# Performance work log

Hardware: AMD Instinct MI355X
Metric: run time of the kernel (lower is better)

Reference implementation:

```python
import jax, jax.numpy as jnp
import numpy as np

B, S, D, H = 8, 1024, 1024, 16
DH = D // H
LN_EPS = 1e-5


def setup_inputs() -> dict:
    key = jax.random.key(0)
    ks = jax.random.split(key, 12)
    lim = 1.0 / np.sqrt(D)
    u = lambda k, shp: jax.random.uniform(k, shp, jnp.float32, -lim, lim)
    return {
        "x": jax.random.normal(ks[0], (B, S, D), jnp.float32),
        "Wq": u(ks[1], (D, D)), "bq": u(ks[2], (D,)),
        "Wk": u(ks[3], (D, D)), "bk": u(ks[4], (D,)),
        "Wv": u(ks[5], (D, D)), "bv": u(ks[6], (D,)),
        "Wo": u(ks[7], (D, D)), "bo": u(ks[8], (D,)),
        "gamma": jnp.ones((D,), jnp.float32),
        "beta": jnp.zeros((D,), jnp.float32),
        "num_head": H,
    }


def reference(x, Wq, bq, Wk, bk, Wv, bv, Wo, bo, gamma, beta, num_head):
    b, s, d = x.shape
    dh = d // num_head
    # projections (torch Linear: y = x @ W.T + b)
    Q = x @ Wq.T + bq
    K = x @ Wk.T + bk
    V = x @ Wv.T + bv
    # faithful raw row-major reshape [B, S, D] -> [B*H, S, DH] (as in the
    # original .view, which does NOT do a proper head split/transpose)
    Q = Q.reshape(b * num_head, -1, dh)
    K = K.reshape(b * num_head, -1, dh)
    V = V.reshape(b * num_head, -1, dh)
    scale = dh ** (-0.5)
    scores = jnp.einsum('bqd,bkd->bqk', Q, K) * scale  # [B*H, S, S]
    alpha = jax.nn.softmax(scores, axis=-1)
    context = jnp.einsum('bqk,bkd->bqd', alpha, V)
    context = context.reshape(b, -1, dh * num_head)
    out = context @ Wo.T + bo
    # dropout is identity in eval mode
    out = out + x
    mu = jnp.mean(out, axis=-1, keepdims=True)
    var = jnp.var(out, axis=-1, keepdims=True)
    out = (out - mu) * jax.lax.rsqrt(var + LN_EPS) * gamma + beta
    return out, alpha
```

## Files before the change

kernel.cpp:

```cpp
#include <hip/hip_runtime.h>
#include <stdint.h>
#include <math.h>

typedef __bf16 bf16_t;
typedef float f32x4 __attribute__((ext_vector_type(4)));
typedef __bf16 bf16x8 __attribute__((ext_vector_type(8)));
typedef __bf16 bf16x4 __attribute__((ext_vector_type(4)));

#define D_ 1024
#define M_ 8192

__device__ __forceinline__ f32x4 mfma16(bf16x8 a, bf16x8 b, f32x4 c) {
  return __builtin_amdgcn_mfma_f32_16x16x32_bf16(a, b, c, 0, 0, 0);
}

__device__ __forceinline__ void gl_lds16(const bf16_t* g, bf16_t* l) {
  __builtin_amdgcn_global_load_lds(
      (const __attribute__((address_space(1))) unsigned int*)g,
      (__attribute__((address_space(3))) unsigned int*)l, 16, 0, 0);
}

__global__ __launch_bounds__(256) void cvt_all(
    const float* __restrict__ x,
    const float* __restrict__ w0, const float* __restrict__ w1,
    const float* __restrict__ w2, const float* __restrict__ w3,
    bf16_t* __restrict__ xb,
    bf16_t* __restrict__ d0, bf16_t* __restrict__ d1,
    bf16_t* __restrict__ d2, bf16_t* __restrict__ d3) {
  int b = blockIdx.x;
  const float* s;
  bf16_t* d;
  int i;
  if (b < 4096) {
    s = x; d = xb; i = b * 256 + threadIdx.x;
  } else {
    int g = b - 4096;
    int which = g >> 9;
    s = which == 0 ? w0 : which == 1 ? w1 : which == 2 ? w2 : w3;
    d = which == 0 ? d0 : which == 1 ? d1 : which == 2 ? d2 : d3;
    i = (g & 511) * 256 + threadIdx.x;
  }
  const f32x4* p = (const f32x4*)(s + (size_t)i * 8);
  f32x4 a = p[0], bb = p[1];
  bf16x8 o;
  o[0] = (bf16_t)a.x; o[1] = (bf16_t)a.y; o[2] = (bf16_t)a.z; o[3] = (bf16_t)a.w;
  o[4] = (bf16_t)bb.x; o[5] = (bf16_t)bb.y; o[6] = (bf16_t)bb.z; o[7] = (bf16_t)bb.w;
  *(bf16x8*)(d + (size_t)i * 8) = o;
}

#define LDSB(e) (*(const bf16x8*)(Sm + (e)))

#define STG2(b, kt)                                                          \
  {                                                                          \
    _Pragma("unroll") for (int c = 0; c < 4; ++c) {                          \
      gl_lds16(A + (size_t)(m0 + c * 64 + srow) * 1024 + (kt) * 64 + scol,   \
               Sm + (b) * 32768 + c * 4096 + tid * 8);                       \
      gl_lds16(Wsel + (size_t)(n0 + c * 64 + srow) * 1024 + (kt) * 64 + scol,\
               Sm + (b) * 32768 + 16384 + c * 4096 + tid * 8);               \
    }                                                                        \
  }

__global__ __launch_bounds__(512) void gemm_qkv2(
    const bf16_t* __restrict__ A,
    const bf16_t* __restrict__ Wq, const bf16_t* __restrict__ Wk,
    const bf16_t* __restrict__ Wv,
    const float* __restrict__ bq, const float* __restrict__ bk,
    const float* __restrict__ bv,
    bf16_t* __restrict__ Oq, bf16_t* __restrict__ Ok, bf16_t* __restrict__ Ov) {
  __shared__ bf16_t Sm[65536];

  const int tid = threadIdx.x;
  const int l = tid & 63, w = tid >> 6;
  const int wm = w >> 2, wn = w & 3;
  const int lr = l & 15, lg = l >> 4;

  int wg = blockIdx.x;
  int xcd = wg & 7, local = wg >> 3;
  int bm = xcd * 4 + (local & 3);
  int bnid = local >> 2;
  int which = bnid >> 2;
  const bf16_t* Wsel = which == 0 ? Wq : (which == 1 ? Wk : Wv);
  const float* bias = which == 0 ? bq : (which == 1 ? bk : bv);
  bf16_t* O = which == 0 ? Oq : (which == 1 ? Ok : Ov);
  const float scale = which == 0 ? 0.18033688f : 1.0f;
  const int m0 = bm * 256, n0 = (bnid & 3) * 256;

  const int scol = ((l & 7) ^ ((l >> 3) & 7)) * 8;
  const int srow = w * 8 + (l >> 3);

  const int rdA = (wm * 128 + lr) * 64 + (lg ^ (lr & 7)) * 8;
  const int rdB = 16384 + (wn * 64 + lr) * 64 + (lg ^ (lr & 7)) * 8;

  f32x4 acc[8][4] = {};

  STG2(0, 0)
  asm volatile("s_waitcnt vmcnt(0)" ::: "memory");
  __builtin_amdgcn_sched_barrier(0);
  __builtin_amdgcn_s_barrier();

  int cur = 0;
  for (int kt = 0; kt < 16; ++kt) {
    if (kt < 15) STG2(cur ^ 1, kt + 1)
    const int bb = cur * 32768;
    bf16x8 bfr[4][2];
#pragma unroll
    for (int fn = 0; fn < 4; ++fn) {
      bfr[fn][0] = LDSB(bb + rdB + fn * 1024);
      bfr[fn][1] = LDSB((bb + rdB + fn * 1024) ^ 32);
    }
#pragma unroll
    for (int fm = 0; fm < 8; ++fm) {
      bf16x8 a0 = LDSB(bb + rdA + fm * 1024);
      bf16x8 a1 = LDSB((bb + rdA + fm * 1024) ^ 32);
#pragma unroll
      for (int fn = 0; fn < 4; ++fn) {
        acc[fm][fn] = mfma16(a0, bfr[fn][0], acc[fm][fn]);
        acc[fm][fn] = mfma16(a1, bfr[fn][1], acc[fm][fn]);
      }
    }
    asm volatile("s_waitcnt vmcnt(0)" ::: "memory");
    __builtin_amdgcn_sched_barrier(0);
    __builtin_amdgcn_s_barrier();
    cur ^= 1;
  }

#pragma unroll
  for (int fn = 0; fn < 4; ++fn) {
    int col = n0 + wn * 64 + fn * 16 + lr;
    float bb2 = bias[col];
#pragma unroll
    for (int fm = 0; fm < 8; ++fm) {
      int row = m0 + wm * 128 + fm * 16 + lg * 4;
      bf16_t* op = O + (size_t)row * 1024 + col;
#pragma unroll
      for (int r = 0; r < 4; ++r)
        op[(size_t)r * 1024] = (bf16_t)((acc[fm][fn][r] + bb2) * scale);
    }
  }
}

__device__ __forceinline__ void gemm_core(const bf16_t* __restrict__ A,
                                          const bf16_t* __restrict__ W,
                                          int m0, int n0,
                                          bf16_t* As, bf16_t* Bs,
                                          f32x4 acc[4][4]) {
  const int t = threadIdx.x;
  const int l = t & 63, w = t >> 6;
  const int wr = w >> 1, wc = w & 1;
  const int lr = l & 15, lg = l >> 4;
  const int srow = t >> 2;
  const int scol = (t & 3) * 8;
  const bf16_t* gA0 = A + (size_t)(m0 + srow) * D_ + scol;
  const bf16_t* gA1 = A + (size_t)(m0 + 64 + srow) * D_ + scol;
  const bf16_t* gB0 = W + (size_t)(n0 + srow) * D_ + scol;
  const bf16_t* gB1 = W + (size_t)(n0 + 64 + srow) * D_ + scol;

  for (int k0 = 0; k0 < D_; k0 += 32) {
    gl_lds16(gA0 + k0, As + t * 8);
    gl_lds16(gA1 + k0, As + 2048 + t * 8);
    gl_lds16(gB0 + k0, Bs + t * 8);
    gl_lds16(gB1 + k0, Bs + 2048 + t * 8);
    __syncthreads();
    bf16x8 af[4], bfr[4];
#pragma unroll
    for (int i = 0; i < 4; ++i)
      af[i] = *(const bf16x8*)(As + (wr * 64 + i * 16 + lr) * 32 + lg * 8);
#pragma unroll
    for (int i = 0; i < 4; ++i)
      bfr[i] = *(const bf16x8*)(Bs + (wc * 64 + i * 16 + lr) * 32 + lg * 8);
#pragma unroll
    for (int mi = 0; mi < 4; ++mi)
#pragma unroll
      for (int ni = 0; ni < 4; ++ni)
        acc[mi][ni] = mfma16(af[mi], bfr[ni], acc[mi][ni]);
    __syncthreads();
  }
}

__global__ __launch_bounds__(256) void gemm_proj(
    const bf16_t* __restrict__ A, const bf16_t* __restrict__ W,
    const float* __restrict__ bias, const float* __restrict__ xres,
    float* __restrict__ O) {
  __shared__ bf16_t As[128 * 32], Bs[128 * 32];
  int m0 = blockIdx.y * 128, n0 = blockIdx.x * 128;
  f32x4 acc[4][4] = {};
  gemm_core(A, W, m0, n0, As, Bs, acc);
  int t = threadIdx.x, l = t & 63, w = t >> 6;
  int wr = w >> 1, wc = w & 1, lr = l & 15, lg = l >> 4;
#pragma unroll
  for (int mi = 0; mi < 4; ++mi) {
#pragma unroll
    for (int ni = 0; ni < 4; ++ni) {
      int col = n0 + wc * 64 + ni * 16 + lr;
      float bb = bias[col];
      int row = m0 + wr * 64 + mi * 16 + lg * 4;
#pragma unroll
      for (int r = 0; r < 4; ++r) {
        size_t idx = (size_t)(row + r) * D_ + col;
        O[idx] = acc[mi][ni][r] + bb + xres[idx];
      }
    }
  }
}

__global__ __launch_bounds__(256) void transpose_v(const bf16_t* __restrict__ V,
                                                   bf16_t* __restrict__ Vt) {
  __shared__ float sT[128 * 33];
  int bh = blockIdx.x >> 3, st = blockIdx.x & 7;
  int s0 = st * 128;
  int t = threadIdx.x;
  const bf16_t* src = V + (size_t)bh * 65536 + (size_t)s0 * 64;
  int li = t >> 3, lc = t & 7;
#pragma unroll
  for (int p = 0; p < 4; ++p) {
    int row = p * 32 + li;
    f32x4 v = *(const f32x4*)(src + (size_t)row * 64 + lc * 8);
    float* dst = &sT[row * 33 + lc * 4];
    dst[0] = v[0]; dst[1] = v[1]; dst[2] = v[2]; dst[3] = v[3];
  }
  __syncthreads();
  int sc = t & 15, dh0 = t >> 4;
  bf16_t* dstb = Vt + (size_t)bh * 65536;
#pragma unroll
  for (int p = 0; p < 4; ++p) {
    int dh = dh0 + p * 16;
    bf16x8 o;
#pragma unroll
    for (int j = 0; j < 8; ++j) {
      int s = sc * 8 + j;
      o[j] = ((const bf16_t*)&sT[s * 33 + (dh >> 1)])[dh & 1];
    }
    *(bf16x8*)(dstb + (size_t)dh * 1024 + s0 + sc * 8) = o;
  }
}

#define SP_STRIDE 1064
__global__ __launch_bounds__(512, 4) void attn_kernel(
    const bf16_t* __restrict__ Q, const bf16_t* __restrict__ K,
    const bf16_t* __restrict__ Vt, float* __restrict__ alpha,
    bf16_t* __restrict__ ctx) {
  __shared__ bf16_t sP[32][SP_STRIDE];
  __shared__ float sRS[8][32];
  __shared__ float sL[32];

  int id = blockIdx.x;
  int g = id >> 3, x = id & 7;
  int qt = g & 31;
  int bh = ((g >> 5) << 3) | x;
  int q0 = qt * 32;

  const bf16_t* Qb = Q + (size_t)bh * 65536;
  const bf16_t* Kb = K + (size_t)bh * 65536;
  const bf16_t* Vb = Vt + (size_t)bh * 65536;
  float* Ab = alpha + (size_t)bh * 1048576 + (size_t)q0 * 1024;

  int t = threadIdx.x, l = t & 63, w = t >> 6;
  int lr = l & 15, lg = l >> 4;

  bf16x8 qa[2][2];
#pragma unroll
  for (int mi = 0; mi < 2; ++mi)
#pragma unroll
    for (int kk = 0; kk < 2; ++kk)
      qa[mi][kk] = *(const bf16x8*)(Qb + (size_t)(q0 + mi * 16 + lr) * 64 + kk * 32 + lg * 8);

  float pa0 = 0.f, pa1 = 0.f;
#pragma unroll
  for (int tt = 0; tt < 8; ++tt) {
    int n0 = w * 128 + tt * 16;
    bf16x8 kb0 = *(const bf16x8*)(Kb + (size_t)(n0 + lr) * 64 + lg * 8);
    bf16x8 kb1 = *(const bf16x8*)(Kb + (size_t)(n0 + lr) * 64 + 32 + lg * 8);
    f32x4 a0 = {0.f, 0.f, 0.f, 0.f};
    f32x4 a1 = {0.f, 0.f, 0.f, 0.f};
    a0 = mfma16(kb0, qa[0][0], a0);
    a0 = mfma16(kb1, qa[0][1], a0);
    a1 = mfma16(kb0, qa[1][0], a1);
    a1 = mfma16(kb1, qa[1][1], a1);
    bf16x4 w0, w1;
#pragma unroll
    for (int r = 0; r < 4; ++r) {
      float e0 = exp2f(a0[r]);
      float e1 = exp2f(a1[r]);
      pa0 += e0; pa1 += e1;
      w0[r] = (bf16_t)e0;
      w1[r] = (bf16_t)e1;
    }
    *(bf16x4*)&sP[lr][n0 + lg * 4] = w0;
    *(bf16x4*)&sP[16 + lr][n0 + lg * 4] = w1;
  }
  pa0 += __shfl_xor(pa0, 16); pa0 += __shfl_xor(pa0, 32);
  pa1 += __shfl_xor(pa1, 16); pa1 += __shfl_xor(pa1, 32);
  if (l < 16) {
    sRS[w][lr] = pa0;
    sRS[w][16 + lr] = pa1;
  }
  __syncthreads();
  if (t < 32) {
    float s = 0.f;
#pragma unroll
    for (int ww = 0; ww < 8; ++ww) s += sRS[ww][t];
    sL[t] = 1.0f / s;
  }
  __syncthreads();

  {
    int wm = w >> 2, wn = w & 3;
    f32x4 acc = {0.f, 0.f, 0.f, 0.f};
    const bf16_t* vp = Vb + (size_t)(wn * 16 + lr) * 1024 + lg * 8;
    const bf16_t* pp = &sP[wm * 16 + lr][lg * 8];
    int arow = t >> 4, acol = (t & 15) * 4;
    float inv = sL[arow];
    const bf16_t* ap = &sP[arow][acol];
    float* aout = Ab + (size_t)arow * 1024 + acol;
#pragma unroll 4
    for (int n0 = 0; n0 < 1024; n0 += 64) {
      bf16x8 ea0 = *(const bf16x8*)(pp + n0);
      bf16x8 vb0 = *(const bf16x8*)(vp + n0);
      acc = mfma16(ea0, vb0, acc);
      bf16x8 ea1 = *(const bf16x8*)(pp + n0 + 32);
      bf16x8 vb1 = *(const bf16x8*)(vp + n0 + 32);
      acc = mfma16(ea1, vb1, acc);
      bf16x4 p = *(const bf16x4*)(ap + n0);
      f32x4 o;
      o[0] = (float)p[0] * inv;
      o[1] = (float)p[1] * inv;
      o[2] = (float)p[2] * inv;
      o[3] = (float)p[3] * inv;
      __builtin_nontemporal_store(o, (f32x4*)(aout + n0));
    }
    bf16_t* cp = ctx + (size_t)bh * 65536 + (size_t)(q0 + wm * 16 + lg * 4) * 64 + wn * 16 + lr;
#pragma unroll
    for (int r = 0; r < 4; ++r)
      cp[(size_t)r * 64] = (bf16_t)(acc[r] * sL[wm * 16 + lg * 4 + r]);
  }
}

__global__ __launch_bounds__(256) void ln_kernel(float* __restrict__ io,
                                                 const float* __restrict__ gamma,
                                                 const float* __restrict__ beta) {
  int row = blockIdx.x;
  int t = threadIdx.x;
  float* p = io + (size_t)row * 1024;
  f32x4 v = *(const f32x4*)(p + t * 4);
  float s = v[0] + v[1] + v[2] + v[3];
  float s2 = v[0] * v[0] + v[1] * v[1] + v[2] * v[2] + v[3] * v[3];
#pragma unroll
  for (int off = 1; off <= 32; off <<= 1) {
    s += __shfl_xor(s, off);
    s2 += __shfl_xor(s2, off);
  }
  __shared__ float ps[4], ps2[4];
  int w = t >> 6, l = t & 63;
  if (l == 0) { ps[w] = s; ps2[w] = s2; }
  __syncthreads();
  float S = ps[0] + ps[1] + ps[2] + ps[3];
  float S2 = ps2[0] + ps2[1] + ps2[2] + ps2[3];
  float mu = S * (1.f / 1024.f);
  float var = S2 * (1.f / 1024.f) - mu * mu;
  float rs = rsqrtf(var + 1e-5f);
  f32x4 g = *(const f32x4*)(gamma + t * 4);
  f32x4 b = *(const f32x4*)(beta + t * 4);
  f32x4 o;
  o[0] = (v[0] - mu) * rs * g[0] + b[0];
  o[1] = (v[1] - mu) * rs * g[1] + b[1];
  o[2] = (v[2] - mu) * rs * g[2] + b[2];
  o[3] = (v[3] - mu) * rs * g[3] + b[3];
  *(f32x4*)(p + t * 4) = o;
}

extern "C" void kernel_launch(void* const* d_in, const int* in_sizes, int n_in,
                              void* d_out, int out_size, void* d_ws, size_t ws_size,
                              hipStream_t stream) {
  const float* x = (const float*)d_in[0];
  const float* Wq = (const float*)d_in[1];
  const float* bq = (const float*)d_in[2];
  const float* Wk = (const float*)d_in[3];
  const float* bk = (const float*)d_in[4];
  const float* Wv = (const float*)d_in[5];
  const float* bv = (const float*)d_in[6];
  const float* Wo = (const float*)d_in[7];
  const float* bo = (const float*)d_in[8];
  const float* gamma = (const float*)d_in[9];
  const float* beta = (const float*)d_in[10];

  char* ws = (char*)d_ws;
  size_t off = 0;
  bf16_t* xb = (bf16_t*)(ws + off);  off += (size_t)M_ * D_ * 2;
  bf16_t* Wqb = (bf16_t*)(ws + off); off += (size_t)D_ * D_ * 2;
  bf16_t* Wkb = (bf16_t*)(ws + off); off += (size_t)D_ * D_ * 2;
  bf16_t* Wvb = (bf16_t*)(ws + off); off += (size_t)D_ * D_ * 2;
  bf16_t* Wob = (bf16_t*)(ws + off); off += (size_t)D_ * D_ * 2;
  bf16_t* Qb = (bf16_t*)(ws + off);  off += (size_t)M_ * D_ * 2;
  bf16_t* Kb = (bf16_t*)(ws + off);  off += (size_t)M_ * D_ * 2;
  bf16_t* Vb = (bf16_t*)(ws + off);  off += (size_t)M_ * D_ * 2;
  bf16_t* Vtb = (bf16_t*)(ws + off); off += (size_t)M_ * D_ * 2;
  bf16_t* ctxb = (bf16_t*)(ws + off); off += (size_t)M_ * D_ * 2;

  float* out0 = (float*)d_out;
  float* alpha = out0 + (size_t)M_ * D_;

  cvt_all<<<6144, 256, 0, stream>>>(x, Wq, Wk, Wv, Wo, xb, Wqb, Wkb, Wvb, Wob);

  gemm_qkv2<<<384, 512, 0, stream>>>(xb, Wqb, Wkb, Wvb, bq, bk, bv, Qb, Kb, Vb);
  transpose_v<<<1024, 256, 0, stream>>>(Vb, Vtb);
  attn_kernel<<<4096, 512, 0, stream>>>(Qb, Kb, Vtb, alpha, ctxb);
  gemm_proj<<<dim3(8, 64), 256, 0, stream>>>(ctxb, Wob, bo, x, out0);
  ln_kernel<<<8192, 256, 0, stream>>>(out0, gamma, beta);
}
```

Measured before the change: 331.0 us.

## Share a 128x256 double-buffered GEMM core between QKV and output projection

The QKV GEMM tile shrinks from 256x256 to 128x256, doubling the grid to 768 workgroups and cutting LDS use and accumulator registers. The output projection moves off its simple single-buffered 128x128 kernel onto the same swizzled, double-buffered 128x256 core with XCD-aware block mapping, 512 threads and a 256-block grid. The aim is better CU occupancy and latency hiding in QKV and better load/compute overlap in the projection. In exchange, QKV re-reads the weight tiles more often per output.

```diff
diff --git a/kernel.cpp b/kernel.cpp
--- a/kernel.cpp
+++ b/kernel.cpp
@@ -50,15 +50,60 @@
 
 #define LDSB(e) (*(const bf16x8*)(Sm + (e)))
 
-#define STG2(b, kt)                                                          \
-  {                                                                          \
-    _Pragma("unroll") for (int c = 0; c < 4; ++c) {                          \
-      gl_lds16(A + (size_t)(m0 + c * 64 + srow) * 1024 + (kt) * 64 + scol,   \
-               Sm + (b) * 32768 + c * 4096 + tid * 8);                       \
-      gl_lds16(Wsel + (size_t)(n0 + c * 64 + srow) * 1024 + (kt) * 64 + scol,\
-               Sm + (b) * 32768 + 16384 + c * 4096 + tid * 8);               \
-    }                                                                        \
-  }
+#define STG26(b, kt)                                                          \
+  {                                                                           \
+    _Pragma("unroll") for (int c = 0; c < 2; ++c)                             \
+        gl_lds16(Ap + (size_t)(m0 + c * 64 + srow) * 1024 + (kt) * 64 + scol, \
+                 Sm + (b) * 24576 + c * 4096 + tid * 8);                      \
+    _Pragma("unroll") for (int c = 0; c < 4; ++c)                             \
+        gl_lds16(Bp + (size_t)(n0 + c * 64 + srow) * 1024 + (kt) * 64 + scol, \
+                 Sm + (b) * 24576 + 8192 + c * 4096 + tid * 8);               \
+  }
+
+__device__ __forceinline__ void core_128x256(const bf16_t* __restrict__ Ap,
+                                             const bf16_t* __restrict__ Bp,
+                                             int m0, int n0, bf16_t* Sm,
+                                             f32x4 acc[4][4]) {
+  const int tid = threadIdx.x;
+  const int l = tid & 63, w = tid >> 6;
+  const int wm = w >> 2, wn = w & 3;
+  const int lr = l & 15, lg = l >> 4;
+  const int scol = ((l & 7) ^ ((l >> 3) & 7)) * 8;
+  const int srow = tid >> 3;
+  const int rdA = (wm * 64 + lr) * 64 + (lg ^ (lr & 7)) * 8;
+  const int rdB = 8192 + (wn * 64 + lr) * 64 + (lg ^ (lr & 7)) * 8;
+
+  STG26(0, 0)
+  asm volatile("s_waitcnt vmcnt(0)" ::: "memory");
+  __builtin_amdgcn_sched_barrier(0);
+  __builtin_amdgcn_s_barrier();
+
+  int cur = 0;
+  for (int kt = 0; kt < 16; ++kt) {
+    if (kt < 15) STG26(cur ^ 1, kt + 1)
+    const int bb = cur * 24576;
+    bf16x8 bfr[4][2];
+#pragma unroll
+    for (int fn = 0; fn < 4; ++fn) {
+      bfr[fn][0] = LDSB(bb + rdB + fn * 1024);
+      bfr[fn][1] = LDSB((bb + rdB + fn * 1024) ^ 32);
+    }
+#pragma unroll
+    for (int fm = 0; fm < 4; ++fm) {
+      bf16x8 a0 = LDSB(bb + rdA + fm * 1024);
+      bf16x8 a1 = LDSB((bb + rdA + fm * 1024) ^ 32);
+#pragma unroll
+      for (int fn = 0; fn < 4; ++fn) {
+        acc[fm][fn] = mfma16(a0, bfr[fn][0], acc[fm][fn]);
+        acc[fm][fn] = mfma16(a1, bfr[fn][1], acc[fm][fn]);
+      }
+    }
+    asm volatile("s_waitcnt vmcnt(0)" ::: "memory");
+    __builtin_amdgcn_sched_barrier(0);
+    __builtin_amdgcn_s_barrier();
+    cur ^= 1;
+  }
+}
 
 __global__ __launch_bounds__(512) void gemm_qkv2(
     const bf16_t* __restrict__ A,
@@ -67,70 +112,33 @@
     const float* __restrict__ bq, const float* __restrict__ bk,
     const float* __restrict__ bv,
     bf16_t* __restrict__ Oq, bf16_t* __restrict__ Ok, bf16_t* __restrict__ Ov) {
-  __shared__ bf16_t Sm[65536];
-
-  const int tid = threadIdx.x;
-  const int l = tid & 63, w = tid >> 6;
-  const int wm = w >> 2, wn = w & 3;
-  const int lr = l & 15, lg = l >> 4;
+  __shared__ bf16_t Sm[49152];
 
   int wg = blockIdx.x;
   int xcd = wg & 7, local = wg >> 3;
-  int bm = xcd * 4 + (local & 3);
-  int bnid = local >> 2;
+  int bm = xcd * 8 + (local & 7);
+  int bnid = local >> 3;
   int which = bnid >> 2;
   const bf16_t* Wsel = which == 0 ? Wq : (which == 1 ? Wk : Wv);
   const float* bias = which == 0 ? bq : (which == 1 ? bk : bv);
   bf16_t* O = which == 0 ? Oq : (which == 1 ? Ok : Ov);
   const float scale = which == 0 ? 0.18033688f : 1.0f;
-  const int m0 = bm * 256, n0 = (bnid & 3) * 256;
-
-  const int scol = ((l & 7) ^ ((l >> 3) & 7)) * 8;
-  const int srow = w * 8 + (l >> 3);
-
-  const int rdA = (wm * 128 + lr) * 64 + (lg ^ (lr & 7)) * 8;
-  const int rdB = 16384 + (wn * 64 + lr) * 64 + (lg ^ (lr & 7)) * 8;
-
-  f32x4 acc[8][4] = {};
-
-  STG2(0, 0)
-  asm volatile("s_waitcnt vmcnt(0)" ::: "memory");
-  __builtin_amdgcn_sched_barrier(0);
-  __builtin_amdgcn_s_barrier();
-
-  int cur = 0;
-  for (int kt = 0; kt < 16; ++kt) {
-    if (kt < 15) STG2(cur ^ 1, kt + 1)
-    const int bb = cur * 32768;
-    bf16x8 bfr[4][2];
-#pragma unroll
-    for (int fn = 0; fn < 4; ++fn) {
-      bfr[fn][0] = LDSB(bb + rdB + fn * 1024);
-      bfr[fn][1] = LDSB((bb + rdB + fn * 1024) ^ 32);
-    }
-#pragma unroll
-    for (int fm = 0; fm < 8; ++fm) {
-      bf16x8 a0 = LDSB(bb + rdA + fm * 1024);
-      bf16x8 a1 = LDSB((bb + rdA + fm * 1024) ^ 32);
-#pragma unroll
-      for (int fn = 0; fn < 4; ++fn) {
-        acc[fm][fn] = mfma16(a0, bfr[fn][0], acc[fm][fn]);
-        acc[fm][fn] = mfma16(a1, bfr[fn][1], acc[fm][fn]);
-      }
-    }
-    asm volatile("s_waitcnt vmcnt(0)" ::: "memory");
-    __builtin_amdgcn_sched_barrier(0);
-    __builtin_amdgcn_s_barrier();
-    cur ^= 1;
-  }
-
+  const int m0 = bm * 128, n0 = (bnid & 3) * 256;
+
+  f32x4 acc[4][4] = {};
+  core_128x256(A, Wsel, m0, n0, Sm, acc);
+
+  const int tid = threadIdx.x;
+  const int l = tid & 63, w = tid >> 6;
+  const int wm = w >> 2, wn = w & 3;
+  const int lr = l & 15, lg = l >> 4;
 #pragma unroll
   for (int fn = 0; fn < 4; ++fn) {
     int col = n0 + wn * 64 + fn * 16 + lr;
     float bb2 = bias[col];
 #pragma unroll
-    for (int fm = 0; fm < 8; ++fm) {
-      int row = m0 + wm * 128 + fm * 16 + lg * 4;
+    for (int fm = 0; fm < 4; ++fm) {
+      int row = m0 + wm * 64 + fm * 16 + lg * 4;
       bf16_t* op = O + (size_t)row * 1024 + col;
 #pragma unroll
       for (int r = 0; r < 4; ++r)
@@ -139,65 +147,36 @@
   }
 }
 
-__device__ __forceinline__ void gemm_core(const bf16_t* __restrict__ A,
-                                          const bf16_t* __restrict__ W,
-                                          int m0, int n0,
-                                          bf16_t* As, bf16_t* Bs,
-                                          f32x4 acc[4][4]) {
-  const int t = threadIdx.x;
-  const int l = t & 63, w = t >> 6;
-  const int wr = w >> 1, wc = w & 1;
-  const int lr = l & 15, lg = l >> 4;
-  const int srow = t >> 2;
-  const int scol = (t & 3) * 8;
-  const bf16_t* gA0 = A + (size_t)(m0 + srow) * D_ + scol;
-  const bf16_t* gA1 = A + (size_t)(m0 + 64 + srow) * D_ + scol;
-  const bf16_t* gB0 = W + (size_t)(n0 + srow) * D_ + scol;
-  const bf16_t* gB1 = W + (size_t)(n0 + 64 + srow) * D_ + scol;
-
-  for (int k0 = 0; k0 < D_; k0 += 32) {
-    gl_lds16(gA0 + k0, As + t * 8);
-    gl_lds16(gA1 + k0, As + 2048 + t * 8);
-    gl_lds16(gB0 + k0, Bs + t * 8);
-    gl_lds16(gB1 + k0, Bs + 2048 + t * 8);
-    __syncthreads();
-    bf16x8 af[4], bfr[4];
-#pragma unroll
-    for (int i = 0; i < 4; ++i)
-      af[i] = *(const bf16x8*)(As + (wr * 64 + i * 16 + lr) * 32 + lg * 8);
-#pragma unroll
-    for (int i = 0; i < 4; ++i)
-      bfr[i] = *(const bf16x8*)(Bs + (wc * 64 + i * 16 + lr) * 32 + lg * 8);
-#pragma unroll
-    for (int mi = 0; mi < 4; ++mi)
-#pragma unroll
-      for (int ni = 0; ni < 4; ++ni)
-        acc[mi][ni] = mfma16(af[mi], bfr[ni], acc[mi][ni]);
-    __syncthreads();
-  }
-}
-
-__global__ __launch_bounds__(256) void gemm_proj(
+__global__ __launch_bounds__(512) void gemm_proj2(
     const bf16_t* __restrict__ A, const bf16_t* __restrict__ W,
     const float* __restrict__ bias, const float* __restrict__ xres,
-    float* __restrict__ O) {
-  __shared__ bf16_t As[128 * 32], Bs[128 * 32];
-  int m0 = blockIdx.y * 128, n0 = blockIdx.x * 128;
+    float* __restrict__ Out) {
+  __shared__ bf16_t Sm[49152];
+
+  int wg = blockIdx.x;
+  int xcd = wg & 7, local = wg >> 3;
+  int bm = xcd * 8 + (local & 7);
+  int bn = local >> 3;
+  const int m0 = bm * 128, n0 = bn * 256;
+
   f32x4 acc[4][4] = {};
-  gemm_core(A, W, m0, n0, As, Bs, acc);
-  int t = threadIdx.x, l = t & 63, w = t >> 6;
-  int wr = w >> 1, wc = w & 1, lr = l & 15, lg = l >> 4;
-#pragma unroll
-  for (int mi = 0; mi < 4; ++mi) {
-#pragma unroll
-    for (int ni = 0; ni < 4; ++ni) {
-      int col = n0 + wc * 64 + ni * 16 + lr;
-      float bb = bias[col];
-      int row = m0 + wr * 64 + mi * 16 + lg * 4;
+  core_128x256(A, W, m0, n0, Sm, acc);
+
+  const int tid = threadIdx.x;
+  const int l = tid & 63, w = tid >> 6;
+  const int wm = w >> 2, wn = w & 3;
+  const int lr = l & 15, lg = l >> 4;
+#pragma unroll
+  for (int fn = 0; fn < 4; ++fn) {
+    int col = n0 + wn * 64 + fn * 16 + lr;
+    float bb2 = bias[col];
+#pragma unroll
+    for (int fm = 0; fm < 4; ++fm) {
+      int row = m0 + wm * 64 + fm * 16 + lg * 4;
 #pragma unroll
       for (int r = 0; r < 4; ++r) {
-        size_t idx = (size_t)(row + r) * D_ + col;
-        O[idx] = acc[mi][ni][r] + bb + xres[idx];
+        size_t idx = (size_t)(row + r) * 1024 + col;
+        Out[idx] = acc[fm][fn][r] + bb2 + xres[idx];
       }
     }
   }
@@ -401,9 +380,9 @@
 
   cvt_all<<<6144, 256, 0, stream>>>(x, Wq, Wk, Wv, Wo, xb, Wqb, Wkb, Wvb, Wob);
 
-  gemm_qkv2<<<384, 512, 0, stream>>>(xb, Wqb, Wkb, Wvb, bq, bk, bv, Qb, Kb, Vb);
+  gemm_qkv2<<<768, 512, 0, stream>>>(xb, Wqb, Wkb, Wvb, bq, bk, bv, Qb, Kb, Vb);
   transpose_v<<<1024, 256, 0, stream>>>(Vb, Vtb);
   attn_kernel<<<4096, 512, 0, stream>>>(Qb, Kb, Vtb, alpha, ctxb);
-  gemm_proj<<<dim3(8, 64), 256, 0, stream>>>(ctxb, Wob, bo, x, out0);
+  gemm_proj2<<<256, 512, 0, stream>>>(ctxb, Wob, bo, x, out0);
   ln_kernel<<<8192, 256, 0, stream>>>(out0, gamma, beta);
 }
```

After: 318.8 us, median of 2. 1.04x faster.
